# Kernel optimization log

Measured on AMD Instinct MI355X. Metric: run time of the kernel, lower is better.

## Reference

```python
import jax, jax.numpy as jnp
import numpy as np

B, T, D = 2, 4096, 2048
HK, HV = 16, 32            # key heads, value heads (gqa_factor = 2)
AK, UV = 128, 128          # key head dim A, value head dim U
KEY_DIM = HK * AK          # 2048
VALUE_DIM = HV * UV        # 4096
CONV_DIM = 2 * KEY_DIM + VALUE_DIM  # 8192
KCONV = 4
CHUNK = 64
EPS = 1e-6


def setup_inputs() -> dict:
    key = jax.random.key(0)
    ks = jax.random.split(key, 10)
    s = lambda d: 1.0 / np.sqrt(d)
    return {
        "hidden": jax.random.normal(ks[0], (B, T, D), jnp.float32),
        "W_qkv": jax.random.normal(ks[1], (D, CONV_DIM), jnp.float32) * s(D),
        "W_z": jax.random.normal(ks[2], (D, VALUE_DIM), jnp.float32) * s(D),
        "W_b": jax.random.normal(ks[3], (D, HV), jnp.float32) * s(D),
        "W_a": jax.random.normal(ks[4], (D, HV), jnp.float32) * s(D),
        "conv_weight": jax.random.normal(ks[5], (CONV_DIM, KCONV), jnp.float32) * s(KCONV),
        "dt_bias": jnp.ones((HV,), jnp.float32),
        "A_log": jnp.log(jax.random.uniform(ks[6], (HV,), jnp.float32) * 16.0 + 1e-4),
        "norm_w": jnp.ones((UV,), jnp.float32),
        "W_out": jax.random.normal(ks[7], (VALUE_DIM, D), jnp.float32) * s(VALUE_DIM),
    }


def _l2norm(x, eps=1e-6):
    return x * jax.lax.rsqrt((x * x).sum(axis=-1, keepdims=True) + eps)


def _chunk_gated_delta_rule(q, k, v, g, beta, chunk_size=CHUNK):
    # inputs: q,k (B,T,Hv,A) l2-normalized below; v (B,T,Hv,U); g,beta (B,T,Hv)
    q = _l2norm(q)
    k = _l2norm(k)
    q, k, v = [x.transpose(0, 2, 1, 3).astype(jnp.float32) for x in (q, k, v)]
    beta = beta.transpose(0, 2, 1).astype(jnp.float32)
    g = g.transpose(0, 2, 1).astype(jnp.float32)
    Bs, H, Tt, A = k.shape
    U = v.shape[-1]
    pad = (chunk_size - Tt % chunk_size) % chunk_size
    if pad:
        q = jnp.pad(q, ((0, 0), (0, 0), (0, pad), (0, 0)))
        k = jnp.pad(k, ((0, 0), (0, 0), (0, pad), (0, 0)))
        v = jnp.pad(v, ((0, 0), (0, 0), (0, pad), (0, 0)))
        beta = jnp.pad(beta, ((0, 0), (0, 0), (0, pad)))
        g = jnp.pad(g, ((0, 0), (0, 0), (0, pad)))
    total = Tt + pad
    J = total // chunk_size
    q = q * (A ** -0.5)
    vb = v * beta[..., None]
    kb = k * beta[..., None]
    rs = lambda x, d: x.reshape(Bs, H, J, chunk_size, d)
    qj, kj, kbj = rs(q, A), rs(k, A), rs(kb, A)
    vbj = rs(vb, U)
    gj = jnp.cumsum(g.reshape(Bs, H, J, chunk_size), axis=-1)
    tril = jnp.tril(jnp.ones((chunk_size, chunk_size), jnp.float32))
    decay = jnp.exp((gj[..., :, None] - gj[..., None, :]) * tril) * tril
    upper = jnp.triu(jnp.ones((chunk_size, chunk_size), bool))
    attn = -(jnp.einsum('BHJLA,BHJMA->BHJLM', kbj, kj) * decay)
    attn = jnp.where(upper, 0.0, attn)

    def correction_step(i, a):  # sequential UT transform over rows
        row = a[..., i, :]
        return a.at[..., i, :].set(row + jnp.einsum('...j,...jk->...k', row, a))

    attn = jax.lax.fori_loop(1, chunk_size, correction_step, attn)
    attn = attn + jnp.eye(chunk_size, dtype=jnp.float32)
    v_corr = jnp.einsum('BHJLM,BHJMU->BHJLU', attn, vbj)
    k_cd = jnp.einsum('BHJLM,BHJMA->BHJLA', attn, kbj * jnp.exp(gj)[..., None])
    upper1 = jnp.triu(jnp.ones((chunk_size, chunk_size), bool), k=1)

    def chunk_step(st, j):  # st: (B,H,A,U) recurrent state
        qc, kc = qj[:, :, j], kj[:, :, j]
        vc, gc, kcd = v_corr[:, :, j], gj[:, :, j], k_cd[:, :, j]
        dm = decay[:, :, j]
        intra = jnp.einsum('BHLA,BHMA->BHLM', qc, kc) * dm
        intra = jnp.where(upper1, 0.0, intra)
        v_new = vc - jnp.einsum('BHLA,BHAU->BHLU', kcd, st)
        inter = jnp.exp(gc)[..., None] * jnp.einsum('BHLA,BHAU->BHLU', qc, st)
        out_c = inter + jnp.einsum('BHLM,BHMU->BHLU', intra, v_new)
        k_dec = kc * jnp.exp(gc[:, :, -1:] - gc)[..., None]
        st = st * jnp.exp(gc[:, :, -1])[..., None, None] + jnp.einsum('BHMA,BHMU->BHAU', k_dec, v_new)
        return st, out_c

    st0 = jnp.zeros((Bs, H, A, U), jnp.float32)
    _, outs = jax.lax.scan(chunk_step, st0, jnp.arange(J))
    out = outs.transpose(1, 2, 0, 3, 4).reshape(Bs, H, total, U)[:, :, :Tt]
    return out.transpose(0, 2, 1, 3)  # (B,T,H,U)


def _forward(hidden, W_qkv, W_z, W_b, W_a, conv_weight, dt_bias, A_log, norm_w, W_out):
    Bs, Tl, _ = hidden.shape
    mixed = (hidden @ W_qkv).transpose(0, 2, 1)  # (B, C, T)
    z = hidden @ W_z                              # (B, T, value_dim)
    b = hidden @ W_b                              # (B, T, Hv)
    a = hidden @ W_a                              # (B, T, Hv)
    # causal depthwise conv1d (kernel KCONV) + SiLU
    xp = jnp.pad(mixed, ((0, 0), (0, 0), (KCONV - 1, 0)))
    conv = sum(conv_weight[None, :, kk:kk + 1] * xp[:, :, kk:kk + Tl] for kk in range(KCONV))
    mixed = jax.nn.silu(conv).transpose(0, 2, 1)  # (B, T, C)
    q, k, v = jnp.split(mixed, [KEY_DIM, 2 * KEY_DIM], axis=-1)
    q = q.reshape(Bs, Tl, HK, AK)
    k = k.reshape(Bs, Tl, HK, AK)
    v = v.reshape(Bs, Tl, HV, UV)
    beta = jax.nn.sigmoid(b)
    g = -jnp.exp(A_log.astype(jnp.float32)) * jax.nn.softplus(a.astype(jnp.float32) + dt_bias)
    gqa = HV // HK
    q = jnp.repeat(q, gqa, axis=2)  # matches broadcast_to+reshape interleaving
    k = jnp.repeat(k, gqa, axis=2)
    core = _chunk_gated_delta_rule(q, k, v, g, beta)  # (B,T,Hv,U)
    # gated RMSNorm per value head (Mamba2/Qwen3-Next style: gate then norm)
    x = core.reshape(-1, UV)
    zf = z.reshape(-1, UV).astype(jnp.float32)
    xg = x * jax.nn.silu(zf)
    normed = norm_w * (xg * jax.lax.rsqrt((xg * xg).mean(-1, keepdims=True) + EPS))
    return normed.reshape(Bs, Tl, VALUE_DIM).astype(hidden.dtype) @ W_out


def reference(hidden, W_qkv, W_z, W_b, W_a, conv_weight, dt_bias, A_log, norm_w, W_out):
    return _forward(hidden, W_qkv, W_z, W_b, W_a, conv_weight, dt_bias, A_log, norm_w, W_out)
```

## Files before the change

### kernel.cpp

```cpp
#include <hip/hip_runtime.h>

#define B_   2
#define T_   4096
#define D_   2048
#define HV_  32
#define AK_  128
#define UV_  128
#define KD_  2048
#define VD_  4096
#define CD_  8192
#define CHK  64
#define NCH  (T_/CHK)

typedef __attribute__((ext_vector_type(4))) float  f32x4;
typedef __attribute__((ext_vector_type(8))) short  short8;
typedef __attribute__((ext_vector_type(4))) short  short4b;
typedef __attribute__((ext_vector_type(8))) unsigned short u16x8;
typedef __attribute__((ext_vector_type(4))) unsigned short u16x4;

__device__ __forceinline__ float bf2f(unsigned short u) {
  return __uint_as_float(((unsigned)u) << 16);
}
__device__ __forceinline__ unsigned short f2bf(float f) {
  unsigned u = __float_as_uint(f);
  return (unsigned short)((u + 0x7fffu + ((u >> 16) & 1u)) >> 16);
}
__device__ __forceinline__ void gload16(const void* g, void* l) {
  __builtin_amdgcn_global_load_lds((const __attribute__((address_space(1))) void*)g,
                                   (__attribute__((address_space(3))) void*)l, 16, 0, 0);
}

__global__ __launch_bounds__(256) void k_transpose(const float* __restrict__ src,
                                                   unsigned short* __restrict__ dst,
                                                   int K, int N) {
  __shared__ float tile[32][33];
  int k0 = blockIdx.x * 32, n0 = blockIdx.y * 32;
  int tx = threadIdx.x, ty = threadIdx.y;
  #pragma unroll
  for (int i = 0; i < 32; i += 8)
    tile[ty + i][tx] = src[(size_t)(k0 + ty + i) * N + n0 + tx];
  __syncthreads();
  #pragma unroll
  for (int i = 0; i < 32; i += 8)
    dst[(size_t)(n0 + ty + i) * K + k0 + tx] = f2bf(tile[tx][ty + i]);
}

__device__ __forceinline__ void storeC(float* p, float v) { *p = v; }
__device__ __forceinline__ void storeC(unsigned short* p, float v) { *p = f2bf(v); }

template <bool AGL, typename CT>
__global__ __launch_bounds__(256, 3) void k_gemm(const void* __restrict__ Av,
                                                 const unsigned short* __restrict__ BT,
                                                 CT* __restrict__ C, int N, int K) {
  __shared__ __attribute__((aligned(16))) short As[128 * 64];
  __shared__ __attribute__((aligned(16))) short Bs[128 * 64];
  const int tid  = threadIdx.x;
  const int bid  = blockIdx.x;
  const int tb   = bid & 63;
  const size_t bm = (size_t)(8 * (tb & 7) + (tb >> 3)) * 128;
  const size_t bn = (size_t)(bid >> 6) * 128;
  const int lane = tid & 63;
  const int wave = tid >> 6;
  const int wm = (wave >> 1) * 64;
  const int wn = (wave & 1) * 64;
  const int fr = lane & 15;
  const int kg = lane >> 4;
  const int lr = lane >> 3, lc8 = (lane & 7) * 8;
  const short* gb = (const short*)BT + (bn + wave * 32 + lr) * (size_t)K + lc8;
  short* lB = &Bs[wave * 32 * 64];
  const short* gab = (const short*)Av + (bm + wave * 32 + lr) * (size_t)K + lc8;
  short* lA = &As[wave * 32 * 64];

  f32x4 acc[4][4];
  #pragma unroll
  for (int i = 0; i < 4; ++i)
    #pragma unroll
    for (int j2 = 0; j2 < 4; ++j2) acc[i][j2] = (f32x4){0.f, 0.f, 0.f, 0.f};

  for (int kt = 0; kt < K; kt += 64) {
    __syncthreads();
    #pragma unroll
    for (int p = 0; p < 4; ++p)
      gload16(gb + kt + (size_t)(8 * p) * K, lB + (8 * p) * 64);
    if constexpr (AGL) {
      #pragma unroll
      for (int p = 0; p < 4; ++p)
        gload16(gab + kt + (size_t)(8 * p) * K, lA + (8 * p) * 64);
    } else {
      const float* Ag = (const float*)Av + bm * (size_t)K;
      #pragma unroll
      for (int s = 0; s < 8; ++s) {
        int ch = s * 256 + tid;
        int r = ch >> 4, c4 = (ch & 15) * 4;
        float4 v = *(const float4*)(Ag + (size_t)r * K + kt + c4);
        short4b sv = { (short)f2bf(v.x), (short)f2bf(v.y), (short)f2bf(v.z), (short)f2bf(v.w) };
        *(short4b*)&As[r * 64 + c4] = sv;
      }
    }
    __syncthreads();
    #pragma unroll
    for (int kk = 0; kk < 2; ++kk) {
      short8 af[4], bfr[4];
      #pragma unroll
      for (int mi = 0; mi < 4; ++mi) af[mi] = *(const short8*)&As[(wm + mi*16 + fr)*64 + kk*32 + kg*8];
      #pragma unroll
      for (int ni = 0; ni < 4; ++ni) bfr[ni] = *(const short8*)&Bs[(wn + ni*16 + fr)*64 + kk*32 + kg*8];
      #pragma unroll
      for (int mi = 0; mi < 4; ++mi)
        #pragma unroll
        for (int ni = 0; ni < 4; ++ni)
          acc[mi][ni] = __builtin_amdgcn_mfma_f32_16x16x32_bf16(af[mi], bfr[ni], acc[mi][ni], 0, 0, 0);
    }
  }
  #pragma unroll
  for (int mi = 0; mi < 4; ++mi)
    #pragma unroll
    for (int ni = 0; ni < 4; ++ni) {
      size_t row = bm + wm + mi * 16 + kg * 4;
      size_t col = bn + wn + ni * 16 + fr;
      #pragma unroll
      for (int e = 0; e < 4; ++e) storeC(&C[(row + e) * (size_t)N + col], acc[mi][ni][e]);
    }
}

__global__ __launch_bounds__(256) void k_beta_g(const float* __restrict__ hidden,
                                                const float* __restrict__ Wb,
                                                const float* __restrict__ Wa,
                                                const float* __restrict__ dt_bias,
                                                const float* __restrict__ A_log,
                                                float* __restrict__ betab,
                                                float* __restrict__ gbuf,
                                                unsigned short* __restrict__ hidb) {
  const int tid = threadIdx.x;
  const int r = tid >> 5, hh = tid & 31;
  const size_t bt = (size_t)blockIdx.x * 8 + r;
  const float* hrow = hidden + bt * D_;
  float sb = 0.f, sa = 0.f;
  for (int d = 0; d < D_; ++d) {
    float hv = hrow[d];
    sb += hv * Wb[d * 32 + hh];
    sa += hv * Wa[d * 32 + hh];
  }
  unsigned short* hb = hidb + bt * D_ + hh * 64;
  #pragma unroll
  for (int d2 = 0; d2 < 64; d2 += 8) {
    float4 v0 = *(const float4*)(hrow + hh * 64 + d2);
    float4 v1 = *(const float4*)(hrow + hh * 64 + d2 + 4);
    u16x8 o = { f2bf(v0.x), f2bf(v0.y), f2bf(v0.z), f2bf(v0.w),
                f2bf(v1.x), f2bf(v1.y), f2bf(v1.z), f2bf(v1.w) };
    *(u16x8*)(hb + d2) = o;
  }
  float beta = 1.f / (1.f + __expf(-sb));
  float xg = sa + dt_bias[hh];
  float sp = (xg > 20.f) ? xg : log1pf(__expf(xg));
  float g = -__expf(A_log[hh]) * sp;
  int b = (int)(bt >> 12);
  int t = (int)(bt & (T_ - 1));
  size_t o = ((size_t)b * HV_ + hh) * T_ + t;
  betab[o] = beta;
  gbuf[o] = g;
}

__global__ __launch_bounds__(256) void k_qkv(const unsigned short* __restrict__ mqk,
                                             const float* __restrict__ cw,
                                             unsigned short* __restrict__ qn,
                                             unsigned short* __restrict__ kn) {
  const int row = blockIdx.x;
  const int b = row >> 12, t = row & (T_ - 1);
  const int tid = threadIdx.x;
  const int c0 = tid * 16;
  float4 w[16];
  #pragma unroll
  for (int e = 0; e < 16; ++e) w[e] = *(const float4*)&cw[(size_t)(c0 + e) * 4];
  float acc[16];
  #pragma unroll
  for (int e = 0; e < 16; ++e) acc[e] = 0.f;
  #pragma unroll
  for (int p = 0; p < 4; ++p) {
    int ts = t - 3 + p;
    if (ts < 0) continue;
    const unsigned short* src = mqk + (size_t)(b * T_ + ts) * 4096 + c0;
    u16x8 v0 = *(const u16x8*)src;
    u16x8 v1 = *(const u16x8*)(src + 8);
    #pragma unroll
    for (int e = 0; e < 8; ++e) {
      acc[e]     += bf2f(v0[e]) * ((const float*)&w[e])[p];
      acc[8 + e] += bf2f(v1[e]) * ((const float*)&w[8 + e])[p];
    }
  }
  float s = 0.f;
  #pragma unroll
  for (int e = 0; e < 16; ++e) {
    float x = acc[e];
    x = x / (1.f + __expf(-x));
    acc[e] = x;
    s += x * x;
  }
  s += __shfl_xor(s, 1); s += __shfl_xor(s, 2); s += __shfl_xor(s, 4);
  float sc = rsqrtf(s + 1e-6f);
  bool isq = (c0 < KD_);
  if (isq) sc *= 0.08838834764831845f;
  int ch = isq ? c0 : (c0 - KD_);
  int hk = ch >> 7, cc = ch & 127;
  unsigned short* dst = (isq ? qn : kn) + ((size_t)(b * 16 + hk) * T_ + t) * 128 + cc;
  u16x8 o0, o1;
  #pragma unroll
  for (int e = 0; e < 8; ++e) { o0[e] = f2bf(acc[e] * sc); o1[e] = f2bf(acc[8 + e] * sc); }
  *(u16x8*)dst = o0;
  *(u16x8*)(dst + 8) = o1;
}

__global__ __launch_bounds__(256) void k_prep(const unsigned short* __restrict__ kn,
                                              const float* __restrict__ gbuf,
                                              const float* __restrict__ betab,
                                              unsigned short* __restrict__ Tg,
                                              unsigned short* __restrict__ knT,
                                              float* __restrict__ gjc) {
  __shared__ __attribute__((aligned(16))) unsigned short kl[CHK][136];
  __shared__ float L[CHK][65];
  __shared__ float W1[CHK][65];
  __shared__ float gj[CHK], bet[CHK];
  const int tid = threadIdx.x;
  const int blk = blockIdx.x;
  const int j = blk & 63, h = (blk >> 6) & 31, b = blk >> 11;
  const int hk = h >> 1;
  const int t0 = j * CHK;
  const int lane = tid & 63, wv = tid >> 6;
  const int fr = lane & 15, kg = lane >> 4;
  const int ty = tid >> 4, tx = tid & 15;

  const unsigned short* ksrc = kn + ((size_t)(b * 16 + hk) * T_ + t0) * 128;
  #pragma unroll
  for (int p = 0; p < 4; ++p) {
    int id = p * 256 + tid;
    int r = id >> 4, c = (id & 15) * 8;
    *(u16x8*)&kl[r][c] = *(const u16x8*)(ksrc + (size_t)r * 128 + c);
  }
  if (tid < 64) {
    float gval = gbuf[((size_t)b * HV_ + h) * T_ + t0 + tid];
    #pragma unroll
    for (int off = 1; off < 64; off <<= 1) {
      float o = __shfl_up(gval, off);
      if (tid >= off) gval += o;
    }
    gj[tid] = gval;
    gjc[((size_t)(b * HV_ + h) * NCH + j) * 64 + tid] = gval;
    bet[tid] = betab[((size_t)b * HV_ + h) * T_ + t0 + tid];
  }
  __syncthreads();

  if ((h & 1) == 0) {
    unsigned short* kd = knT + ((size_t)(b * 16 + hk) * NCH + j) * 8192;
    int a = tid >> 1, l0 = (tid & 1) * 32;
    u16x8 o[4];
    #pragma unroll
    for (int i = 0; i < 32; ++i) ((unsigned short*)o)[i] = kl[l0 + i][a];
    #pragma unroll
    for (int p = 0; p < 4; ++p) *(u16x8*)(kd + a * 64 + l0 + p * 8) = o[p];
  }

  {
    const int s0 = 16 * wv;
    f32x4 ag[4];
    #pragma unroll
    for (int mt = 0; mt < 4; ++mt) ag[mt] = (f32x4){0.f, 0.f, 0.f, 0.f};
    #pragma unroll
    for (int ks = 0; ks < 4; ++ks) {
      short8 af = *(const short8*)&kl[s0 + fr][ks * 32 + kg * 8];
      #pragma unroll
      for (int mt = 0; mt < 4; ++mt) {
        short8 bfv = *(const short8*)&kl[mt * 16 + fr][ks * 32 + kg * 8];
        ag[mt] = __builtin_amdgcn_mfma_f32_16x16x32_bf16(af, bfv, ag[mt], 0, 0, 0);
      }
    }
    #pragma unroll
    for (int mt = 0; mt < 4; ++mt)
      #pragma unroll
      for (int e = 0; e < 4; ++e) {
        int l = s0 + kg * 4 + e, m = mt * 16 + fr;
        L[l][m] = (l > m) ? (-bet[l] * ag[mt][e] * __expf(gj[l] - gj[m])) : 0.f;
      }
  }
  __syncthreads();
  for (int i = tid; i < CHK * CHK; i += 256) { int l = i >> 6, m = i & 63; W1[l][m] = L[l][m]; }
  __syncthreads();

  #pragma unroll
  for (int dk = 1; dk <= 5; ++dk) {
    const int p2 = 1 << (dk - 1);
    float s4[4][4];
    #pragma unroll
    for (int i = 0; i < 4; ++i)
      #pragma unroll
      for (int c = 0; c < 4; ++c) s4[i][c] = 0.f;
    {
      const int hi = 16 * wv + 15 - p2;
      for (int jm = p2; jm <= hi; ++jm) {
        float wl[4], wr[4];
        #pragma unroll
        for (int i = 0; i < 4; ++i) wl[i] = W1[ty * 4 + i][jm];
        #pragma unroll
        for (int c = 0; c < 4; ++c) wr[c] = W1[jm][tx * 4 + c];
        #pragma unroll
        for (int i = 0; i < 4; ++i)
          #pragma unroll
          for (int c = 0; c < 4; ++c) s4[i][c] += wl[i] * wr[c];
      }
    }
    __syncthreads();
    #pragma unroll
    for (int i = 0; i < 4; ++i)
      #pragma unroll
      for (int c = 0; c < 4; ++c) W1[ty * 4 + i][tx * 4 + c] = s4[i][c];
    __syncthreads();
    float pu[4][4];
    #pragma unroll
    for (int i = 0; i < 4; ++i)
      #pragma unroll
      for (int c = 0; c < 4; ++c) pu[i][c] = L[ty * 4 + i][tx * 4 + c] + W1[ty * 4 + i][tx * 4 + c];
    {
      const int hi = 16 * wv + 14;
      for (int jm = p2 * 2; jm <= hi; ++jm) {
        float pl[4], wr[4];
        #pragma unroll
        for (int i = 0; i < 4; ++i) pl[i] = L[ty * 4 + i][jm];
        #pragma unroll
        for (int c = 0; c < 4; ++c) wr[c] = W1[jm][tx * 4 + c];
        #pragma unroll
        for (int i = 0; i < 4; ++i)
          #pragma unroll
          for (int c = 0; c < 4; ++c) pu[i][c] += pl[i] * wr[c];
      }
    }
    __syncthreads();
    #pragma unroll
    for (int i = 0; i < 4; ++i)
      #pragma unroll
      for (int c = 0; c < 4; ++c) L[ty * 4 + i][tx * 4 + c] = pu[i][c];
    __syncthreads();
  }
  unsigned short* td = Tg + (size_t)blk * 4096;
  #pragma unroll
  for (int pp = 0; pp < 2; ++pp) {
    int id = pp * 256 + tid;
    int l = id >> 3, m8 = (id & 7) * 8;
    u16x8 o;
    #pragma unroll
    for (int e = 0; e < 8; ++e) {
      float v = L[l][m8 + e] + ((l == m8 + e) ? 1.f : 0.f);
      o[e] = f2bf(v);
    }
    *(u16x8*)(td + (size_t)l * 64 + m8) = o;
  }
}

__global__ __launch_bounds__(256) void k_scan(const unsigned short* __restrict__ qn,
                                              const unsigned short* __restrict__ kn,
                                              const unsigned short* __restrict__ mv,
                                              const unsigned short* __restrict__ Tg,
                                              const unsigned short* __restrict__ knT,
                                              const float* __restrict__ gjc,
                                              const float* __restrict__ betab,
                                              const float* __restrict__ cw,
                                              unsigned short* __restrict__ xout) {
  __shared__ __attribute__((aligned(16))) unsigned short kl[CHK][136];
  __shared__ __attribute__((aligned(16))) unsigned short intr[CHK][72];
  __shared__ float ST[16][132];
  __shared__ __attribute__((aligned(16))) unsigned short SbT[16][136];
  __shared__ __attribute__((aligned(16))) unsigned short vbT[16][72], vnT[16][72], vndT[16][72];
  __shared__ float gj[CHK], bet[CHK], eg[CHK], edec[CHK], beg[CHK];

  const int tid = threadIdx.x;
  const int blk = blockIdx.x;
  const int xcd  = blk & 7;
  const int slot = blk >> 3;
  const int g    = xcd + 8 * (slot >> 4);
  const int wgrp = slot & 15;
  const int b  = g >> 4;
  const int hk = g & 15;
  const int h  = hk * 2 + (wgrp >> 3);
  const int us = wgrp & 7;
  const int u0 = us * 16;
  const int lane = tid & 63, wv = tid >> 6;
  const int fr = lane & 15, kg = lane >> 4;
  const int s0 = 16 * wv;

  const int cvl = tid >> 2, c4 = (tid & 3) * 4;
  float4 wv4[4];
  #pragma unroll
  for (int i = 0; i < 4; ++i)
    wv4[i] = *(const float4*)&cw[(size_t)(2 * KD_ + h * 128 + u0 + c4 + i) * 4];

  for (int i = tid; i < 16 * 132; i += 256) (&ST[0][0])[i] = 0.f;

  const unsigned short* qsrc = qn + (size_t)(b * 16 + hk) * T_ * 128;
  const unsigned short* ksrc = kn + (size_t)(b * 16 + hk) * T_ * 128;
  const unsigned short* tsrc = Tg + (size_t)((b * 32 + h) * 64) * 4096;
  const unsigned short* knsrc = knT + (size_t)(b * 16 + hk) * NCH * 8192;
  const float* gsrc = gjc + (size_t)(b * 32 + h) * 4096;
  const float* bsrc = betab + ((size_t)b * HV_ + h) * T_;

  const int rr = tid >> 4, cc8 = (tid & 15) * 8;

  u16x8 krg[4];
  u16x4 vld[4];
  float g_r = 0.f, b_r = 0.f;

  #pragma unroll
  for (int p = 0; p < 4; ++p) {
    int r = p * 16 + rr;
    krg[p] = *(const u16x8*)(ksrc + (size_t)r * 128 + cc8);
  }
  if (tid < 64) { g_r = gsrc[tid]; b_r = bsrc[tid]; }
  #pragma unroll
  for (int p = 0; p < 4; ++p) {
    int ts = cvl - 3 + p;
    vld[p] = (ts >= 0) ? *(const u16x4*)(mv + (size_t)(b * T_ + ts) * 4096 + h * 128 + u0 + c4)
                       : (u16x4){0, 0, 0, 0};
  }
  #pragma unroll
  for (int p = 0; p < 4; ++p) {
    int r = p * 16 + rr;
    *(u16x8*)&kl[r][cc8] = krg[p];
  }
  if (tid < 64) { gj[tid] = g_r; bet[tid] = b_r; }
  __syncthreads();

  for (int j = 0; j < NCH; ++j) {
    const int t0 = j * CHK;
    short8 kr[2][2], qf[4], tf[2];
    #pragma unroll
    for (int t2 = 0; t2 < 2; ++t2) {
      int a0 = wv * 32 + t2 * 16;
      #pragma unroll
      for (int ks = 0; ks < 2; ++ks)
        kr[t2][ks] = *(const short8*)(knsrc + (size_t)j * 8192 + (a0 + fr) * 64 + ks * 32 + kg * 8);
    }
    #pragma unroll
    for (int ks = 0; ks < 4; ++ks)
      qf[ks] = *(const short8*)(qsrc + (size_t)(t0 + s0 + fr) * 128 + ks * 32 + kg * 8);
    #pragma unroll
    for (int ks = 0; ks < 2; ++ks)
      tf[ks] = *(const short8*)(tsrc + (size_t)j * 4096 + (s0 + fr) * 64 + ks * 32 + kg * 8);
    if (j + 1 < NCH) {
      const int t1 = t0 + CHK;
      #pragma unroll
      for (int p = 0; p < 4; ++p) {
        int r = p * 16 + rr;
        krg[p] = *(const u16x8*)(ksrc + (size_t)(t1 + r) * 128 + cc8);
      }
      if (tid < 64) { g_r = gsrc[(j + 1) * 64 + tid]; b_r = bsrc[t1 + tid]; }
    }
    if (tid < 64) {
      float gl = gj[63];
      float e = __expf(gj[tid]);
      eg[tid] = e;
      edec[tid] = __expf(gl - gj[tid]);
      beg[tid] = bet[tid] * e;
    }
    {
      float a4[4] = {0.f, 0.f, 0.f, 0.f};
      #pragma unroll
      for (int p = 0; p < 4; ++p)
        #pragma unroll
        for (int i = 0; i < 4; ++i) a4[i] += bf2f(vld[p][i]) * ((const float*)&wv4[i])[p];
      float be = bet[cvl];
      #pragma unroll
      for (int i = 0; i < 4; ++i) {
        float x = a4[i];
        x = x / (1.f + __expf(-x)) * be;
        vbT[c4 + i][cvl] = f2bf(x);
      }
    }
    if (j + 1 < NCH) {
      #pragma unroll
      for (int p = 0; p < 4; ++p) {
        int ts = t0 + CHK + cvl - 3 + p;
        vld[p] = *(const u16x4*)(mv + (size_t)(b * T_ + ts) * 4096 + h * 128 + u0 + c4);
      }
    }
    {
      int u = tid >> 4, a8 = (tid & 15) * 8;
      u16x8 o;
      #pragma unroll
      for (int e = 0; e < 8; ++e) o[e] = f2bf(ST[u][a8 + e]);
      *(u16x8*)&SbT[u][a8] = o;
    }
    __syncthreads();

    {
      f32x4 ag[4];
      #pragma unroll
      for (int mt = 0; mt < 4; ++mt) ag[mt] = (f32x4){0.f, 0.f, 0.f, 0.f};
      #pragma unroll
      for (int ks = 0; ks < 4; ++ks) {
        #pragma unroll
        for (int mt = 0; mt < 4; ++mt) {
          short8 bfv = *(const short8*)&kl[mt * 16 + fr][ks * 32 + kg * 8];
          ag[mt] = __builtin_amdgcn_mfma_f32_16x16x32_bf16(qf[ks], bfv, ag[mt], 0, 0, 0);
        }
      }
      #pragma unroll
      for (int mt = 0; mt < 4; ++mt)
        #pragma unroll
        for (int e = 0; e < 4; ++e) {
          int l = s0 + kg * 4 + e, m = mt * 16 + fr;
          float v = (l >= m) ? (ag[mt][e] * __expf(gj[l] - gj[m])) : 0.f;
          intr[l][m] = f2bf(v);
        }
    }
    {
      f32x4 a1 = (f32x4){0.f, 0.f, 0.f, 0.f};
      #pragma unroll
      for (int ks = 0; ks < 4; ++ks) {
        short8 af = *(const short8*)&kl[s0 + fr][ks * 32 + kg * 8];
        short8 bfv = *(const short8*)&SbT[fr][ks * 32 + kg * 8];
        a1 = __builtin_amdgcn_mfma_f32_16x16x32_bf16(af, bfv, a1, 0, 0, 0);
      }
      #pragma unroll
      for (int e = 0; e < 4; ++e) {
        int l = s0 + kg * 4 + e;
        float vm = bf2f(vbT[fr][l]) - beg[l] * a1[e];
        vbT[fr][l] = f2bf(vm);
      }
    }
    __syncthreads();
    {
      f32x4 a2 = (f32x4){0.f, 0.f, 0.f, 0.f};
      #pragma unroll
      for (int ks = 0; ks < 2; ++ks) {
        short8 bfv = *(const short8*)&vbT[fr][ks * 32 + kg * 8];
        a2 = __builtin_amdgcn_mfma_f32_16x16x32_bf16(tf[ks], bfv, a2, 0, 0, 0);
      }
      #pragma unroll
      for (int e = 0; e < 4; ++e) {
        int l = s0 + kg * 4 + e;
        vnT[fr][l]  = f2bf(a2[e]);
        vndT[fr][l] = f2bf(a2[e] * edec[l]);
      }
    }
    __syncthreads();
    {
      f32x4 ai = (f32x4){0.f, 0.f, 0.f, 0.f};
      f32x4 aq = (f32x4){0.f, 0.f, 0.f, 0.f};
      #pragma unroll
      for (int ks = 0; ks < 2; ++ks) {
        short8 af = *(const short8*)&intr[s0 + fr][ks * 32 + kg * 8];
        short8 bfv = *(const short8*)&vnT[fr][ks * 32 + kg * 8];
        ai = __builtin_amdgcn_mfma_f32_16x16x32_bf16(af, bfv, ai, 0, 0, 0);
      }
      #pragma unroll
      for (int ks = 0; ks < 4; ++ks) {
        short8 bfv = *(const short8*)&SbT[fr][ks * 32 + kg * 8];
        aq = __builtin_amdgcn_mfma_f32_16x16x32_bf16(qf[ks], bfv, aq, 0, 0, 0);
      }
      #pragma unroll
      for (int e = 0; e < 4; ++e) {
        int l = s0 + kg * 4 + e;
        float o = eg[l] * aq[e] + ai[e];
        xout[((size_t)(b * T_ + t0 + l) * HV_ + h) * UV_ + u0 + fr] = f2bf(o);
      }
    }
    {
      float egl = eg[63];
      #pragma unroll
      for (int t2 = 0; t2 < 2; ++t2) {
        int a0 = wv * 32 + t2 * 16;
        f32x4 cf;
        #pragma unroll
        for (int e = 0; e < 4; ++e) cf[e] = ST[kg * 4 + e][a0 + fr] * egl;
        #pragma unroll
        for (int ks = 0; ks < 2; ++ks) {
          short8 af = *(const short8*)&vndT[fr][ks * 32 + kg * 8];
          cf = __builtin_amdgcn_mfma_f32_16x16x32_bf16(af, kr[t2][ks], cf, 0, 0, 0);
        }
        #pragma unroll
        for (int e = 0; e < 4; ++e) ST[kg * 4 + e][a0 + fr] = cf[e];
      }
    }
    __syncthreads();
    if (j + 1 < NCH) {
      #pragma unroll
      for (int p = 0; p < 4; ++p) {
        int r = p * 16 + rr;
        *(u16x8*)&kl[r][cc8] = krg[p];
      }
      if (tid < 64) { gj[tid] = g_r; bet[tid] = b_r; }
    }
    __syncthreads();
  }
}

__global__ __launch_bounds__(256) void k_gate_norm(const unsigned short* __restrict__ x,
                                                   const unsigned short* __restrict__ z,
                                                   const float* __restrict__ nw,
                                                   unsigned short* __restrict__ out) {
  const int row = blockIdx.x * 4 + (threadIdx.x >> 6);
  const int lane = threadIdx.x & 63;
  const unsigned short* xp = x + (size_t)row * UV_;
  const unsigned short* zp = z + (size_t)row * UV_;
  float x0 = bf2f(xp[lane]), x1 = bf2f(xp[lane + 64]);
  float z0 = bf2f(zp[lane]), z1 = bf2f(zp[lane + 64]);
  float g0 = x0 * (z0 / (1.f + __expf(-z0)));
  float g1 = x1 * (z1 / (1.f + __expf(-z1)));
  float s = g0 * g0 + g1 * g1;
  #pragma unroll
  for (int off = 32; off > 0; off >>= 1) s += __shfl_xor(s, off);
  float r = rsqrtf(s * (1.f / UV_) + 1e-6f);
  out[(size_t)row * UV_ + lane]      = f2bf(nw[lane] * g0 * r);
  out[(size_t)row * UV_ + lane + 64] = f2bf(nw[lane + 64] * g1 * r);
}

extern "C" void kernel_launch(void* const* d_in, const int* in_sizes, int n_in,
                              void* d_out, int out_size, void* d_ws, size_t ws_size,
                              hipStream_t stream) {
  (void)in_sizes; (void)n_in; (void)out_size; (void)ws_size;
  const float* hidden  = (const float*)d_in[0];
  const float* W_qkv   = (const float*)d_in[1];
  const float* W_z     = (const float*)d_in[2];
  const float* W_b     = (const float*)d_in[3];
  const float* W_a     = (const float*)d_in[4];
  const float* conv_w  = (const float*)d_in[5];
  const float* dt_bias = (const float*)d_in[6];
  const float* A_log   = (const float*)d_in[7];
  const float* norm_w  = (const float*)d_in[8];
  const float* W_out   = (const float*)d_in[9];
  float* out = (float*)d_out;

  const size_t MB = 1048576ull;
  char* w = (char*)d_ws;
  unsigned short* wqkvT = (unsigned short*)(w);
  unsigned short* Tg    = (unsigned short*)(w);
  unsigned short* mqk   = (unsigned short*)(w + 32 * MB);
  unsigned short* xcore = (unsigned short*)(w + 32 * MB);
  unsigned short* mv    = (unsigned short*)(w + 96 * MB);
  unsigned short* normed= (unsigned short*)(w + 96 * MB);
  unsigned short* hidb  = (unsigned short*)(w + 160 * MB);
  unsigned short* qn    = (unsigned short*)(w + 160 * MB);
  unsigned short* zb    = (unsigned short*)(w + 160 * MB);
  unsigned short* knT   = (unsigned short*)(w + 192 * MB);
  unsigned short* kn    = (unsigned short*)(w + 224 * MB);
  unsigned short* wzT   = (unsigned short*)(w + 224 * MB);
  unsigned short* woutT = (unsigned short*)(w + 240 * MB);
  float*          betab = (float*)(w + 288 * MB);
  float*          gbuf  = (float*)(w + 289 * MB);
  float*          gjc   = (float*)(w + 290 * MB);

  k_beta_g<<<dim3(B_ * T_ / 8), 256, 0, stream>>>(hidden, W_b, W_a, dt_bias, A_log, betab, gbuf, hidb);
  k_transpose<<<dim3(D_ / 32, CD_ / 32), dim3(32, 8), 0, stream>>>(W_qkv, wqkvT, D_, CD_);
  k_gemm<true, unsigned short><<<dim3(64 * 32), 256, 0, stream>>>(hidb, wqkvT, mqk, 4096, 2048);
  k_gemm<true, unsigned short><<<dim3(64 * 32), 256, 0, stream>>>(hidb, wqkvT + (size_t)4096 * 2048, mv, 4096, 2048);
  k_qkv<<<dim3(B_ * T_), 256, 0, stream>>>(mqk, conv_w, qn, kn);
  k_prep<<<dim3(B_ * HV_ * NCH), 256, 0, stream>>>(kn, gbuf, betab, Tg, knT, gjc);
  k_scan<<<dim3(B_ * HV_ * 8), 256, 0, stream>>>(qn, kn, mv, Tg, knT, gjc, betab, conv_w, xcore);
  k_transpose<<<dim3(D_ / 32, VD_ / 32), dim3(32, 8), 0, stream>>>(W_z, wzT, D_, VD_);
  k_gemm<false, unsigned short><<<dim3(64 * 32), 256, 0, stream>>>(hidden, wzT, zb, 4096, 2048);
  k_transpose<<<dim3(VD_ / 32, D_ / 32), dim3(32, 8), 0, stream>>>(W_out, woutT, VD_, D_);
  k_gate_norm<<<dim3(B_ * T_ * HV_ / 4), 256, 0, stream>>>(xcore, zb, norm_w, normed);
  k_gemm<true, float><<<dim3(64 * 16), 256, 0, stream>>>(normed, woutT, out, 2048, 4096);
}
```

Baseline: 1.612 ms.

## Add 256x256-tile triple-buffered bf16 GEMM for QKV and output projections

Introduces a new GEMM kernel with 512 threads, 256x256 output tiles, K-step 32, and a three-stage LDS ring buffer filled by async global-to-LDS loads, using XOR-swizzled LDS addresses and setprio around the MFMA bursts. It replaces the 128x128 GEMM for the two QKV projections and the output projection, with the aim of raising arithmetic intensity per tile and overlapping loads with MFMA work. The trade-off is one block per CU with heavy register use, and only 512 or 256 blocks for these GEMM shapes, which can leave the GPU's 256 CUs poorly filled and add tail effects.

After: 1.729 ms. +7.3%, slower.

```diff
diff --git a/kernel.cpp b/kernel.cpp
--- a/kernel.cpp
+++ b/kernel.cpp
@@ -47,6 +47,103 @@
 
 __device__ __forceinline__ void storeC(float* p, float v) { *p = v; }
 __device__ __forceinline__ void storeC(unsigned short* p, float v) { *p = f2bf(v); }
+
+template <typename CT>
+__global__ __launch_bounds__(512, 1) void k_gemm256(const unsigned short* __restrict__ A,
+                                                    const unsigned short* __restrict__ BT,
+                                                    CT* __restrict__ C, int N, int K) {
+  __shared__ __attribute__((aligned(16))) short As[3][256 * 32];
+  __shared__ __attribute__((aligned(16))) short Bs[3][256 * 32];
+  const int tid  = threadIdx.x;
+  const size_t bm = (size_t)blockIdx.x * 256;
+  const size_t bn = (size_t)blockIdx.y * 256;
+  const int lane = tid & 63;
+  const int wid  = tid >> 6;
+  const int wr = wid >> 2, wc = wid & 3;
+  const int fr = lane & 15, kg = lane >> 4;
+
+  const int c0 = wid * 64 + lane;
+  const int r0 = c0 >> 2, s0x = ((c0 & 3) ^ ((r0 >> 1) & 3)) * 8;
+  const int c1 = 512 + c0;
+  const int r1 = c1 >> 2, s1x = ((c1 & 3) ^ ((r1 >> 1) & 3)) * 8;
+  const unsigned short* gA0 = A  + (bm + r0) * (size_t)K + s0x;
+  const unsigned short* gA1 = A  + (bm + r1) * (size_t)K + s1x;
+  const unsigned short* gB0 = BT + (bn + r0) * (size_t)K + s0x;
+  const unsigned short* gB1 = BT + (bn + r1) * (size_t)K + s1x;
+  const int lb0 = wid * 512;
+  const int lb1 = 4096 + lb0;
+
+  int addrA[8], addrB[4];
+  #pragma unroll
+  for (int f = 0; f < 8; ++f) {
+    int ra = wr * 128 + f * 16 + fr;
+    addrA[f] = ra * 32 + ((kg ^ ((ra >> 1) & 3)) * 8);
+  }
+  #pragma unroll
+  for (int g2 = 0; g2 < 4; ++g2) {
+    int rb = wc * 64 + g2 * 16 + fr;
+    addrB[g2] = rb * 32 + ((kg ^ ((rb >> 1) & 3)) * 8);
+  }
+
+  f32x4 acc[8][4];
+  #pragma unroll
+  for (int f = 0; f < 8; ++f)
+    #pragma unroll
+    for (int g2 = 0; g2 < 4; ++g2) acc[f][g2] = (f32x4){0.f, 0.f, 0.f, 0.f};
+
+  const int nt = K >> 5;
+  #pragma unroll
+  for (int t = 0; t < 2; ++t) {
+    const int kt = t * 32;
+    gload16(gA0 + kt, &As[t][lb0]);
+    gload16(gA1 + kt, &As[t][lb1]);
+    gload16(gB0 + kt, &Bs[t][lb0]);
+    gload16(gB1 + kt, &Bs[t][lb1]);
+  }
+
+  int cur = 0;
+  for (int i = 0; i < nt; ++i) {
+    if (i + 1 < nt) { asm volatile("s_waitcnt vmcnt(4)" ::: "memory"); }
+    else            { asm volatile("s_waitcnt vmcnt(0)" ::: "memory"); }
+    __builtin_amdgcn_sched_barrier(0);
+    __builtin_amdgcn_s_barrier();
+    __builtin_amdgcn_sched_barrier(0);
+    if (i + 2 < nt) {
+      const int nb = (cur + 2 >= 3) ? cur - 1 : cur + 2;
+      const int kt = (i + 2) * 32;
+      gload16(gA0 + kt, &As[nb][lb0]);
+      gload16(gA1 + kt, &As[nb][lb1]);
+      gload16(gB0 + kt, &Bs[nb][lb0]);
+      gload16(gB1 + kt, &Bs[nb][lb1]);
+    }
+    {
+      const short* Ab = &As[cur][0];
+      const short* Bb = &Bs[cur][0];
+      short8 bf[4];
+      #pragma unroll
+      for (int g2 = 0; g2 < 4; ++g2) bf[g2] = *(const short8*)&Bb[addrB[g2]];
+      #pragma unroll
+      for (int f = 0; f < 8; ++f) {
+        short8 af = *(const short8*)&Ab[addrA[f]];
+        __builtin_amdgcn_s_setprio(1);
+        #pragma unroll
+        for (int g2 = 0; g2 < 4; ++g2)
+          acc[f][g2] = __builtin_amdgcn_mfma_f32_16x16x32_bf16(af, bf[g2], acc[f][g2], 0, 0, 0);
+        __builtin_amdgcn_s_setprio(0);
+      }
+    }
+    cur = (cur == 2) ? 0 : cur + 1;
+  }
+  #pragma unroll
+  for (int f = 0; f < 8; ++f)
+    #pragma unroll
+    for (int g2 = 0; g2 < 4; ++g2) {
+      size_t row = bm + wr * 128 + f * 16 + kg * 4;
+      size_t col = bn + wc * 64 + g2 * 16 + fr;
+      #pragma unroll
+      for (int e = 0; e < 4; ++e) storeC(&C[(row + e) * (size_t)N + col], acc[f][g2][e]);
+    }
+}
 
 template <bool AGL, typename CT>
 __global__ __launch_bounds__(256, 3) void k_gemm(const void* __restrict__ Av,
@@ -648,8 +745,8 @@
 
   k_beta_g<<<dim3(B_ * T_ / 8), 256, 0, stream>>>(hidden, W_b, W_a, dt_bias, A_log, betab, gbuf, hidb);
   k_transpose<<<dim3(D_ / 32, CD_ / 32), dim3(32, 8), 0, stream>>>(W_qkv, wqkvT, D_, CD_);
-  k_gemm<true, unsigned short><<<dim3(64 * 32), 256, 0, stream>>>(hidb, wqkvT, mqk, 4096, 2048);
-  k_gemm<true, unsigned short><<<dim3(64 * 32), 256, 0, stream>>>(hidb, wqkvT + (size_t)4096 * 2048, mv, 4096, 2048);
+  k_gemm256<unsigned short><<<dim3(32, 16), 512, 0, stream>>>(hidb, wqkvT, mqk, 4096, 2048);
+  k_gemm256<unsigned short><<<dim3(32, 16), 512, 0, stream>>>(hidb, wqkvT + (size_t)4096 * 2048, mv, 4096, 2048);
   k_qkv<<<dim3(B_ * T_), 256, 0, stream>>>(mqk, conv_w, qn, kn);
   k_prep<<<dim3(B_ * HV_ * NCH), 256, 0, stream>>>(kn, gbuf, betab, Tg, knT, gjc);
   k_scan<<<dim3(B_ * HV_ * 8), 256, 0, stream>>>(qn, kn, mv, Tg, knT, gjc, betab, conv_w, xcore);
@@ -657,5 +754,5 @@
   k_gemm<false, unsigned short><<<dim3(64 * 32), 256, 0, stream>>>(hidden, wzT, zb, 4096, 2048);
   k_transpose<<<dim3(VD_ / 32, D_ / 32), dim3(32, 8), 0, stream>>>(W_out, woutT, VD_, D_);
   k_gate_norm<<<dim3(B_ * T_ * HV_ / 4), 256, 0, stream>>>(xcore, zb, norm_w, normed);
-  k_gemm<true, float><<<dim3(64 * 16), 256, 0, stream>>>(normed, woutT, out, 2048, 4096);
-}
+  k_gemm256<float><<<dim3(32, 8), 512, 0, stream>>>(normed, woutT, out, 2048, 4096);
+}
```
